# Kernel tuning notes

Hardware: AMD Instinct MI355X
Metric: run time of the kernel (lower is better)

Reference implementation:

```python
import jax, jax.numpy as jnp
import numpy as np

B, N, K = 4, 1024, 512
HEADS, DH = 8, 64
HID = 2048
KAPPA = 1.0      # kappa_beta
ALPHA = 1e-3     # ffn_alpha (prior weight)
LAM = 1.0        # ffn_lambda_belief
NITER = 2        # ffn_n_iterations
EPS = 1e-8


def _ln(x, g, b):
    m = jnp.mean(x, axis=-1, keepdims=True)
    v = jnp.var(x, axis=-1, keepdims=True)
    return (x - m) * jax.lax.rsqrt(v + 1e-5) * g + b


def _transport(x, phi, G):
    # truncated exp(phi . G) applied to x without materializing (B,N,K,K)
    def Ax(y):
        return jnp.einsum('bng,gkl,bnl->bnk', phi, G, y)
    a1 = Ax(x)
    return x + a1 + 0.5 * Ax(a1)


def setup_inputs() -> dict:
    key = jax.random.key(0)
    ks = jax.random.split(key, 16)
    mu_q = jax.random.normal(ks[0], (B, N, K), dtype=jnp.float32)
    sigma_q = jax.random.uniform(ks[1], (B, N, K), minval=0.5, maxval=1.5, dtype=jnp.float32)
    phi = 0.1 * jax.random.normal(ks[2], (B, N, 3), dtype=jnp.float32)
    A = jax.random.normal(ks[3], (3, K, K), dtype=jnp.float32)
    generators = 0.05 * (A - jnp.transpose(A, (0, 2, 1)))  # antisymmetric Lie generators
    mask = jnp.broadcast_to(jnp.tril(jnp.ones((N, N), dtype=bool)), (B, N, N))  # causal
    mu_prior = jax.random.normal(ks[4], (B, N, K), dtype=jnp.float32)
    s = 0.02
    Wq = s * jax.random.normal(ks[5], (K, K), dtype=jnp.float32)
    Wk = s * jax.random.normal(ks[6], (K, K), dtype=jnp.float32)
    Wv = s * jax.random.normal(ks[7], (K, K), dtype=jnp.float32)
    Wo = s * jax.random.normal(ks[8], (K, K), dtype=jnp.float32)
    g1 = jnp.ones((K,), jnp.float32); be1 = jnp.zeros((K,), jnp.float32)
    g2 = jnp.ones((K,), jnp.float32); be2 = jnp.zeros((K,), jnp.float32)
    W1 = s * jax.random.normal(ks[9], (K, HID), dtype=jnp.float32)
    bh1 = jnp.zeros((HID,), jnp.float32)
    W2 = s * jax.random.normal(ks[10], (HID, K), dtype=jnp.float32)
    bh2 = jnp.zeros((K,), jnp.float32)
    lr = jnp.array(0.1, jnp.float32)  # learnable VFE step size
    return {'mu_q': mu_q, 'sigma_q': sigma_q, 'phi': phi, 'generators': generators,
            'mask': mask, 'mu_prior': mu_prior, 'Wq': Wq, 'Wk': Wk, 'Wv': Wv, 'Wo': Wo,
            'g1': g1, 'be1': be1, 'g2': g2, 'be2': be2,
            'W1': W1, 'bh1': bh1, 'W2': W2, 'bh2': bh2, 'lr': lr}


def reference(mu_q, sigma_q, phi, generators, mask, mu_prior,
              Wq, Wk, Wv, Wo, g1, be1, g2, be2, W1, bh1, W2, bh2, lr):
    # ---- attention sublayer ----
    mu_n = _ln(mu_q, g1, be1)
    mu_g = _transport(mu_n, phi, generators)  # transport to common frame

    def heads(x):  # (B,N,K) -> (B,H,N,Dh)
        return x.reshape(B, N, HEADS, DH).transpose(0, 2, 1, 3)

    q = heads(mu_g @ Wq)
    k = heads(mu_g @ Wk)
    v = heads(mu_g @ Wv)
    # diagonal covariance propagated through linear maps: var_out = sigma @ W^2
    sq = heads(sigma_q @ (Wq * Wq)) + EPS
    sk = heads(sigma_q @ (Wk * Wk)) + EPS

    inv = 1.0 / sq
    # KL(N(k_j,sk_j) || N(q_i,sq_i)) for diagonal Gaussians, decomposed into matmuls
    tr = jnp.einsum('bhid,bhjd->bhij', inv, sk)
    quad = (jnp.sum(q * q * inv, axis=-1)[..., None]
            - 2.0 * jnp.einsum('bhid,bhjd->bhij', q * inv, k)
            + jnp.einsum('bhid,bhjd->bhij', inv, k * k))
    logdet = (jnp.sum(jnp.log(sq), axis=-1)[..., None]
              - jnp.sum(jnp.log(sk), axis=-1)[:, :, None, :])
    kl = 0.5 * (tr + quad - DH + logdet)  # (B,H,N,N)

    scores = jnp.where(mask[:, None, :, :], -kl / KAPPA, -1e9)
    beta = jax.nn.softmax(scores, axis=-1)

    out = jnp.einsum('bhij,bhjd->bhid', beta, v)
    out = out.transpose(0, 2, 1, 3).reshape(B, N, K)
    mu_attn = _transport(out @ Wo, -phi, generators)  # back-transport to local frames
    mu_res = mu_q + mu_attn  # residual (dropout is identity in eval)

    # ---- VFE_dynamic FFN sublayer ----
    mu_n2 = _ln(mu_res, g2, be2)
    beta_m = jnp.mean(beta, axis=1)  # (B,N,N) attention-belief coupling
    h = mu_n2
    for _ in range(NITER):
        drive = jax.nn.gelu(h @ W1 + bh1) @ W2 + bh2
        grad = ALPHA * (h - mu_prior) + LAM * (h - jnp.einsum('bij,bjk->bik', beta_m, h))
        h = h + lr * (drive - grad)
    mu_out = mu_res + (h - mu_n2)

    return (mu_out, sigma_q, phi)
```

## Files before the change

kernel.cpp:

```cpp
#include <hip/hip_runtime.h>
#include <math.h>

#define BB 4
#define NN 1024
#define KK 512
#define HH 8
#define DHh 64
#define HIDd 2048
#define BN (BB*NN)

typedef unsigned short u16;
typedef __attribute__((ext_vector_type(8))) short bf16x8;
typedef __attribute__((ext_vector_type(4))) float f32x4;

__device__ __forceinline__ float gelu_tanh(float x){
    float u = 0.7978845608028654f*(x + 0.044715f*x*x*x);
    u = fminf(fmaxf(u, -15.f), 15.f);
    float t = __expf(2.f*u);
    return x*t/(t+1.f);
}
__device__ __forceinline__ u16 f2bf(float x){
    unsigned int u = __float_as_uint(x);
    unsigned int r = (u + 0x7fffu + ((u>>16)&1u)) >> 16;
    return (u16)r;
}
__device__ __forceinline__ float bf2f(u16 b){
    return __uint_as_float(((unsigned int)b)<<16);
}
__device__ __forceinline__ void gload16(const void* g, void* l){
    __builtin_amdgcn_global_load_lds((__attribute__((address_space(1))) void*)g,
                                     (__attribute__((address_space(3))) void*)l, 16, 0, 0);
}
__device__ __forceinline__ void wsplit(u16* hi, u16* lo, size_t o, float v){
    u16 h = f2bf(v);
    hi[o] = h;
    if (lo) lo[o] = f2bf(v - bf2f(h));
}

__global__ __launch_bounds__(256) void split_t_k(
    const float* __restrict__ src, u16* __restrict__ hi, u16* __restrict__ lo,
    int Kc, int Nc, long sS, long sD, int square)
{
    __shared__ float t[32][33];
    const int n0 = blockIdx.x*32, k0 = blockIdx.y*32, bz = blockIdx.z;
    const float* S = src + (long)bz*sS;
    const int tx = threadIdx.x & 31, ty = threadIdx.x >> 5;
    for (int r = ty; r < 32; r += 8){
        float v = S[(long)(k0+r)*Nc + n0+tx];
        if (square) v *= v;
        t[r][tx] = v;
    }
    __syncthreads();
    for (int r = ty; r < 32; r += 8){
        float v = t[tx][r];
        long o = (long)bz*sD + (long)(n0+r)*Kc + k0 + tx;
        wsplit(hi, lo, o, v);
    }
}

__global__ __launch_bounds__(256) void wmega_k(
    const float* __restrict__ Wq, const float* __restrict__ Wk,
    const float* __restrict__ Wv, const float* __restrict__ Wo,
    const float* __restrict__ W1, const float* __restrict__ W2,
    const float* __restrict__ gen,
    u16* __restrict__ WQKVh, u16* __restrict__ WQKVl, u16* __restrict__ WoTh,
    u16* __restrict__ WSQKh, u16* __restrict__ WSQKl,
    u16* __restrict__ W1Th, u16* __restrict__ W2Th, u16* __restrict__ GFh)
{
    const int z = blockIdx.z;
    const int tid = threadIdx.x;
    if (z == 8){
        if (blockIdx.x >= 48) return;
        const int c0 = blockIdx.x*32, k0 = blockIdx.y*32;
        const int tx = tid&31, ty = tid>>5;
        const int g = c0/KK, l0 = c0%KK;
        for (int r=ty; r<32; r+=8)
            GFh[(size_t)(k0+r)*(3*KK) + c0+tx] =
                f2bf(gen[(size_t)g*KK*KK + (size_t)(k0+r)*KK + l0+tx]);
        return;
    }
    __shared__ float t[32][33];
    const float* src; u16* hi; u16* lo=0; int sq=0;
    int n0, k0, Kc, Nc;
    const size_t KK2 = (size_t)KK*KK;
    if (z < 6){
        if (blockIdx.x >= 16) return;
        n0 = blockIdx.x*32; k0 = blockIdx.y*32; Kc=KK; Nc=KK;
        if      (z==0){ src=Wq; hi=WQKVh;       lo=WQKVl; }
        else if (z==1){ src=Wk; hi=WQKVh+KK2;   lo=WQKVl+KK2; }
        else if (z==2){ src=Wv; hi=WQKVh+2*KK2; lo=WQKVl+2*KK2; }
        else if (z==3){ src=Wo; hi=WoTh; }
        else if (z==4){ src=Wq; hi=WSQKh;       lo=WSQKl; sq=1; }
        else          { src=Wk; hi=WSQKh+KK2;   lo=WSQKl+KK2; sq=1; }
    } else if (z == 6){
        src=W1; hi=W1Th; Kc=KK; Nc=HIDd;
        n0 = blockIdx.x*32; k0 = blockIdx.y*32;
    } else {
        src=W2; hi=W2Th; Kc=HIDd; Nc=KK;
        n0 = blockIdx.y*32; k0 = blockIdx.x*32;
    }
    const int tx=tid&31, ty=tid>>5;
    for (int r=ty;r<32;r+=8){
        float v = src[(long)(k0+r)*Nc + n0+tx];
        if (sq) v*=v;
        t[r][tx]=v;
    }
    __syncthreads();
    for (int r=ty;r<32;r+=8){
        float v = t[tx][r];
        long o = (long)(n0+r)*Kc + k0+tx;
        wsplit(hi, lo, o, v);
    }
}

__global__ __launch_bounds__(256) void gemm_mfma_k(
    const u16* __restrict__ Ah, const u16* __restrict__ Bh,
    float* __restrict__ C, u16* __restrict__ Chi, u16* __restrict__ Clo,
    int M, int Kc, int Nc, int lda,
    long sA, long sB, long sC, const float* __restrict__ bias, int act,
    int swz)
{
    __shared__ u16 shA[3][128*32], shB[3][128*32];
    int bx = blockIdx.x, by = blockIdx.y;
    if (swz){
        int lin = bx + gridDim.x*by;
        int within = lin & 31, st = lin >> 5;
        int stm = gridDim.x >> 3;
        bx = (st % stm)*8 + (within & 7);
        by = (st / stm)*4 + (within >> 3);
    }
    const int m0 = bx*128, n0 = by*128;
    const int bz = blockIdx.z;
    const u16* gAh = Ah + (long)bz*sA;
    const u16* gBh = Bh + (long)bz*sB;
    const int tid = threadIdx.x;
    const int wave = tid >> 6, lane = tid & 63;
    const int quad = lane >> 4, r16 = lane & 15;
    const int wm = (wave>>1)*64, wn = (wave&1)*64;

    f32x4 acc[4][4];
    #pragma unroll
    for (int i=0;i<4;i++)
        #pragma unroll
        for (int j=0;j<4;j++) acc[i][j] = (f32x4){0.f,0.f,0.f,0.f};

    auto stage = [&](int sel, int k0){
        #pragma unroll
        for (int half=0; half<2; ++half){
            int c = half*256 + tid;
            int row = c >> 2;
            int kg = ((c & 3) ^ ((row >> 1) & 3))*8;
            gload16(gAh + (long)(m0+row)*lda + k0 + kg, &shA[sel][c*8]);
            gload16(gBh + (long)(n0+row)*Kc  + k0 + kg, &shB[sel][c*8]);
        }
    };

    const int nsteps = Kc >> 5;
    stage(0, 0);
    if (1 < nsteps) stage(1, 1<<5);
    const int swr = (quad ^ ((r16 >> 1) & 3))*8;
    for (int t = 0; t < nsteps; ++t){
        if (t+1 < nsteps) asm volatile("s_waitcnt vmcnt(4)" ::: "memory");
        else              asm volatile("s_waitcnt vmcnt(0)" ::: "memory");
        __builtin_amdgcn_s_barrier();
        if (t+2 < nsteps) stage((t+2)%3, (t+2)<<5);
        const int rd = t % 3;
        bf16x8 afh[4], bfh[4];
        #pragma unroll
        for (int i=0;i<4;i++){
            afh[i] = *(const bf16x8*)&shA[rd][(wm+i*16+r16)*32 + swr];
            bfh[i] = *(const bf16x8*)&shB[rd][(wn+i*16+r16)*32 + swr];
        }
        #pragma unroll
        for (int i=0;i<4;i++)
            #pragma unroll
            for (int j=0;j<4;j++)
                acc[i][j] = __builtin_amdgcn_mfma_f32_16x16x32_bf16(afh[i], bfh[j], acc[i][j], 0,0,0);
    }
    #pragma unroll
    for (int i=0;i<4;i++){
        #pragma unroll
        for (int j=0;j<4;j++){
            int gc = n0 + wn + j*16 + r16;
            if (gc >= Nc) continue;
            float bv = bias ? bias[gc] : 0.f;
            #pragma unroll
            for (int r=0;r<4;r++){
                long gr = m0 + wm + i*16 + quad*4 + r;
                float v = acc[i][j][r] + bv;
                if (act) v = gelu_tanh(v);
                long o = (long)bz*sC + gr*Nc + gc;
                if (C) C[o] = v;
                if (Chi){ u16 t = f2bf(v); Chi[o] = t; if (Clo) Clo[o] = f2bf(v - bf2f(t)); }
            }
        }
    }
}

template<int NBUF>
__global__ __launch_bounds__(256) void gemm_v3_k(
    const u16* __restrict__ Ah, const u16* __restrict__ Al,
    const u16* __restrict__ Bh, const u16* __restrict__ Bl,
    float* __restrict__ C,
    int M, int Kc, int Nc, int lda,
    long sA, long sB, long sC, int cskip, int swzmode,
    const u16* __restrict__ Ah2, const u16* __restrict__ Al2,
    const u16* __restrict__ Bh2, const u16* __restrict__ Bl2,
    float* __restrict__ C2, int ycut, int Nc2)
{
    __shared__ u16 shA[NBUF][128*32], shB[NBUF][128*32];
    int bx = blockIdx.x, by = blockIdx.y, bz = blockIdx.z;
    if (swzmode == 1){
        int lin = bx + gridDim.x*by;
        int within = lin & 31, st = lin >> 5;
        int stm = gridDim.x >> 3;
        bx = (st % stm)*8 + (within & 7);
        by = (st / stm)*4 + (within >> 3);
    } else if (swzmode == 2){
        int lin = bx + gridDim.x*(by + gridDim.y*bz);
        int xcd = lin & 7, idx = lin >> 3;
        bz = xcd + 8*(idx >> 6);
        int tile = idx & 63;
        bx = tile & 7; by = tile >> 3;
    }
    if (ycut && by >= ycut){
        Ah = Ah2; Al = Al2; Bh = Bh2; Bl = Bl2; C = C2;
        by -= ycut; Nc = Nc2;
    }
    const int m0 = bx*128, n0 = by*128;
    if (cskip == 1 && n0 > m0 + 127) return;
    const u16* gAh = Ah + (long)bz*sA;
    const u16* gAl = Al + (long)bz*sA;
    const u16* gBh = Bh + (long)bz*sB;
    const u16* gBl = Bl + (long)bz*sB;
    const int tid = threadIdx.x;
    const int wave = tid >> 6, lane = tid & 63;
    const int quad = lane >> 4, r16 = lane & 15;
    const int wm = (wave>>1)*64, wn = (wave&1)*64;

    f32x4 acc[4][4];
    #pragma unroll
    for (int i=0;i<4;i++)
        #pragma unroll
        for (int j=0;j<4;j++) acc[i][j] = (f32x4){0.f,0.f,0.f,0.f};

    const int segsteps = Kc >> 5;
    const int nsteps = 3*segsteps;
    auto stage = [&](int sel, int t){
        int seg = (t >= segsteps) + (t >= 2*segsteps);
        int k0 = (t - seg*segsteps) << 5;
        const u16* a = (seg==1) ? gAl : gAh;
        const u16* b = (seg==2) ? gBl : gBh;
        #pragma unroll
        for (int half=0; half<2; ++half){
            int c = half*256 + tid;
            int row = c >> 2;
            int kg = ((c & 3) ^ ((row >> 1) & 3))*8;
            gload16(a + (long)(m0+row)*lda + k0 + kg, &shA[sel][c*8]);
            gload16(b + (long)(n0+row)*Kc  + k0 + kg, &shB[sel][c*8]);
        }
    };

    const int swr = (quad ^ ((r16 >> 1) & 3))*8;
    if constexpr (NBUF == 2){
        stage(0, 0);
        __syncthreads();
        int cur = 0;
        for (int t = 0; t < nsteps; ++t){
            if (t+1 < nsteps) stage(cur^1, t+1);
            bf16x8 afh[4], bfh[4];
            #pragma unroll
            for (int i=0;i<4;i++){
                afh[i] = *(const bf16x8*)&shA[cur][(wm+i*16+r16)*32 + swr];
                bfh[i] = *(const bf16x8*)&shB[cur][(wn+i*16+r16)*32 + swr];
            }
            #pragma unroll
            for (int i=0;i<4;i++)
                #pragma unroll
                for (int j=0;j<4;j++)
                    acc[i][j] = __builtin_amdgcn_mfma_f32_16x16x32_bf16(afh[i], bfh[j], acc[i][j], 0,0,0);
            __syncthreads();
            cur ^= 1;
        }
    } else {
        stage(0, 0);
        if (1 < nsteps) stage(1, 1);
        for (int t = 0; t < nsteps; ++t){
            if (t+1 < nsteps) asm volatile("s_waitcnt vmcnt(4)" ::: "memory");
            else              asm volatile("s_waitcnt vmcnt(0)" ::: "memory");
            __builtin_amdgcn_s_barrier();
            if (t+2 < nsteps) stage((t+2)%3, t+2);
            const int rd = t % 3;
            bf16x8 afh[4], bfh[4];
            #pragma unroll
            for (int i=0;i<4;i++){
                afh[i] = *(const bf16x8*)&shA[rd][(wm+i*16+r16)*32 + swr];
                bfh[i] = *(const bf16x8*)&shB[rd][(wn+i*16+r16)*32 + swr];
            }
            #pragma unroll
            for (int i=0;i<4;i++)
                #pragma unroll
                for (int j=0;j<4;j++)
                    acc[i][j] = __builtin_amdgcn_mfma_f32_16x16x32_bf16(afh[i], bfh[j], acc[i][j], 0,0,0);
        }
    }
    #pragma unroll
    for (int i=0;i<4;i++){
        #pragma unroll
        for (int j=0;j<4;j++){
            int gc = n0 + wn + j*16 + r16;
            if (gc >= Nc) continue;
            #pragma unroll
            for (int r=0;r<4;r++){
                long gr = m0 + wm + i*16 + quad*4 + r;
                if (cskip == 1 && gc > gr) continue;
                long o = (long)bz*sC + gr*Nc + gc;
                C[o] = acc[i][j][r];
            }
        }
    }
}

__global__ __launch_bounds__(256) void tgemm_k(
    const u16* __restrict__ Ahh,
    const u16* __restrict__ GFh,
    const float* __restrict__ phi, float esign,
    float* __restrict__ C, u16* __restrict__ Chi, u16* __restrict__ Clo,
    const float* __restrict__ t_x, const float* __restrict__ t_a1,
    const float* __restrict__ t_res)
{
    __shared__ u16 shA[2][64*64], shB[2][64*64];
    const int m0 = blockIdx.x*64, n0 = blockIdx.y*64;
    const int tid = threadIdx.x;
    const int wave = tid >> 6, lane = tid & 63;
    const int quad = lane >> 4, r16 = lane & 15;
    const int wr = wave*16;

    float ph[3][4];
    #pragma unroll
    for (int sgi=0; sgi<3; ++sgi)
        #pragma unroll
        for (int r=0; r<4; ++r)
            ph[sgi][r] = esign*phi[(size_t)(m0+wr+quad*4+r)*3 + sgi];

    f32x4 acc[4], tot[4];
    #pragma unroll
    for (int j=0;j<4;j++){ acc[j] = (f32x4){0.f,0.f,0.f,0.f}; tot[j] = acc[j]; }

    auto stage = [&](int sel, int t){
        int seg = t >> 3, k0 = (t & 7) << 6;
        #pragma unroll
        for (int rep=0; rep<2; ++rep){
            int c = rep*256 + tid;
            int row = c >> 3;
            int kg = ((c & 7) ^ (row & 7))*8;
            gload16(Ahh + (long)(m0+row)*KK + k0 + kg, &shA[sel][c*8]);
            gload16(GFh + (long)(n0+row)*(3*KK) + seg*KK + k0 + kg, &shB[sel][c*8]);
        }
    };

    stage(0, 0);
    __syncthreads();
    int cur = 0;
    for (int t = 0; t < 24; ++t){
        if (t+1 < 24) stage(cur^1, t+1);
        #pragma unroll
        for (int kk=0; kk<2; ++kk){
            const int s = (((kk<<2)+quad) ^ (r16 & 7))*8;
            bf16x8 af = *(const bf16x8*)&shA[cur][(wr+r16)*64 + s];
            #pragma unroll
            for (int j=0;j<4;j++){
                bf16x8 bh = *(const bf16x8*)&shB[cur][(j*16+r16)*64 + s];
                acc[j] = __builtin_amdgcn_mfma_f32_16x16x32_bf16(af, bh, acc[j], 0,0,0);
            }
        }
        if ((t & 7) == 7){
            int sgi = t >> 3;
            #pragma unroll
            for (int j=0;j<4;j++){
                #pragma unroll
                for (int r=0;r<4;r++) tot[j][r] += ph[sgi][r]*acc[j][r];
                acc[j] = (f32x4){0.f,0.f,0.f,0.f};
            }
        }
        __syncthreads();
        cur ^= 1;
    }
    #pragma unroll
    for (int j=0;j<4;j++){
        int gc = n0 + j*16 + r16;
        #pragma unroll
        for (int r=0;r<4;r++){
            long gr = m0 + wr + quad*4 + r;
            float v = tot[j][r];
            long o = gr*(long)KK + gc;
            if (t_x){
                v = t_x[o] + t_a1[o] + 0.5f*v;
                if (t_res) v += t_res[o];
            }
            if (C) C[o] = v;
            if (Chi){ u16 t2 = f2bf(v); Chi[o] = t2; if (Clo) Clo[o] = f2bf(v - bf2f(t2)); }
        }
    }
}

__global__ __launch_bounds__(256) void gemm64_k(
    const u16* __restrict__ Ah, const u16* __restrict__ Bh,
    float* __restrict__ C, u16* __restrict__ Chi, u16* __restrict__ Clo,
    int M, int Kc, int Nc, int lda,
    long sA, long sB, long sC, const float* __restrict__ bias, int act,
    int ktrim, int swz,
    const float* __restrict__ f_hin, const float* __restrict__ f_bmh,
    const float* __restrict__ f_mup, const float* __restrict__ f_lr,
    u16* __restrict__ f_hh, float* __restrict__ f_hout,
    const float* __restrict__ f_mrb, const float* __restrict__ f_mn2,
    float* __restrict__ f_out, int fmode)
{
    __shared__ u16 shA[2][64*64], shB[2][64*64];
    int bx = blockIdx.x, by = blockIdx.y;
    if (swz){
        int lin = bx + gridDim.x*by;
        int within = lin & 31, st = lin >> 5;
        int stm = gridDim.x >> 3;
        bx = (st % stm)*8 + (within & 7);
        by = (st / stm)*4 + (within >> 3);
    }
    const int m0 = bx*64, n0 = by*64;
    const int bz = blockIdx.z;
    const u16* gA = Ah + (long)bz*sA;
    const u16* gB = Bh + (long)bz*sB;
    const int tid = threadIdx.x;
    const int wave = tid >> 6, lane = tid & 63;
    const int quad = lane >> 4, r16 = lane & 15;
    const int wr = wave*16;
    const int kend = ktrim ? min(Kc, m0 + 64) : Kc;
    const int nsteps = kend >> 6;

    f32x4 acc[4];
    #pragma unroll
    for (int j=0;j<4;j++) acc[j] = (f32x4){0.f,0.f,0.f,0.f};

    auto stage = [&](int sel, int k0){
        #pragma unroll
        for (int rep=0; rep<2; ++rep){
            int c = rep*256 + tid;
            int row = c >> 3;
            int kg = ((c & 7) ^ (row & 7))*8;
            gload16(gA + (long)(m0+row)*lda + k0 + kg, &shA[sel][c*8]);
            gload16(gB + (long)(n0+row)*Kc + k0 + kg, &shB[sel][c*8]);
        }
    };

    stage(0, 0);
    __syncthreads();
    int cur = 0;
    for (int t = 0; t < nsteps; ++t){
        if (t+1 < nsteps) stage(cur^1, (t+1)<<6);
        #pragma unroll
        for (int kk=0; kk<2; ++kk){
            const int s = (((kk<<2)+quad) ^ (r16 & 7))*8;
            bf16x8 af = *(const bf16x8*)&shA[cur][(wr+r16)*64 + s];
            #pragma unroll
            for (int j=0;j<4;j++){
                bf16x8 bh = *(const bf16x8*)&shB[cur][(j*16+r16)*64 + s];
                acc[j] = __builtin_amdgcn_mfma_f32_16x16x32_bf16(af, bh, acc[j], 0,0,0);
            }
        }
        __syncthreads();
        cur ^= 1;
    }
    float lrv = 0.f;
    if (fmode) lrv = *f_lr;
    #pragma unroll
    for (int j=0;j<4;j++){
        int gc = n0 + j*16 + r16;
        float bv = bias ? bias[gc] : 0.f;
        #pragma unroll
        for (int r=0;r<4;r++){
            long gr = m0 + wr + quad*4 + r;
            float v = acc[j][r] + bv;
            if (act) v = gelu_tanh(v);
            long o = (long)bz*sC + gr*Nc + gc;
            if (fmode){
                float hv = f_hin[o];
                float val = hv + lrv*(v - (1e-3f*(hv - f_mup[o]) + (hv - f_bmh[o])));
                if (fmode == 1){ f_hout[o] = val; f_hh[o] = f2bf(val); }
                else           { f_out[o] = f_mrb[o] + val - f_mn2[o]; }
            } else {
                if (C) C[o] = v;
                if (Chi){ u16 t = f2bf(v); Chi[o] = t; if (Clo) Clo[o] = f2bf(v - bf2f(t)); }
            }
        }
    }
}

__global__ __launch_bounds__(256) void ln_k(
    const float* __restrict__ x, const float* __restrict__ g,
    const float* __restrict__ be, float* __restrict__ y,
    u16* __restrict__ yh16,
    const float* __restrict__ sg, u16* __restrict__ sgh, u16* __restrict__ sgl,
    float* __restrict__ osig, const float* __restrict__ phi, float* __restrict__ ophi)
{
    __shared__ float sh[8];
    const int r = blockIdx.x, tid = threadIdx.x;
    const float* xr = x + (long)r*KK;
    float2 v = *(const float2*)(xr + tid*2);
    float s = v.x+v.y, s2 = v.x*v.x+v.y*v.y;
    #pragma unroll
    for (int o=32;o>0;o>>=1){ s += __shfl_down(s,o); s2 += __shfl_down(s2,o); }
    if ((tid&63)==0){ sh[tid>>6]=s; sh[4+(tid>>6)]=s2; }
    __syncthreads();
    s  = sh[0]+sh[1]+sh[2]+sh[3];
    s2 = sh[4]+sh[5]+sh[6]+sh[7];
    const float mean = s*(1.f/KK);
    const float var  = s2*(1.f/KK) - mean*mean;
    const float rs = rsqrtf(var + 1e-5f);
    float2 gg = *(const float2*)(g + tid*2);
    float2 bb = *(const float2*)(be + tid*2);
    float ox = (v.x-mean)*rs*gg.x + bb.x;
    float oy = (v.y-mean)*rs*gg.y + bb.y;
    long o = (long)r*KK + tid*2;
    *(float2*)(y + o) = make_float2(ox, oy);
    if (yh16){ yh16[o] = f2bf(ox); yh16[o+1] = f2bf(oy); }
    if (sgh){
        float2 sv = *(const float2*)(sg + o);
        wsplit(sgh, sgl, o,   sv.x);
        wsplit(sgh, sgl, o+1, sv.y);
        if (osig) *(float2*)(osig + o) = sv;
    }
    if (ophi && tid < 3) ophi[(size_t)r*3 + tid] = phi[(size_t)r*3 + tid];
}

__global__ __launch_bounds__(512) void prepvt_k(
    const float* __restrict__ QKV, const float* __restrict__ SQSK,
    u16* __restrict__ CFh, u16* __restrict__ CFl,
    u16* __restrict__ KSh, u16* __restrict__ KSl, float* __restrict__ dvec,
    u16* __restrict__ VTh)
{
    __shared__ float t[64][65];
    const int bx = blockIdx.x;
    const int tid = threadIdx.x;
    if (bx < BN){
        const int bn = bx;
        const int b = bn / NN, n = bn % NN;
        const int h = tid >> 6, d = tid & 63;
        float q  = QKV[(size_t)bn*1536 + h*DHh + d];
        float k  = QKV[(size_t)bn*1536 + KK + h*DHh + d];
        float sq = SQSK[(size_t)bn*1024 + h*DHh + d] + 1e-8f;
        float sk = SQSK[(size_t)bn*1024 + KK + h*DHh + d] + 1e-8f;
        float inv = 1.f/sq;
        float nqi = -2.f*q*inv;
        float skk = sk + k*k;
        const size_t base = ((size_t)(h*BB + b)*NN + n)*128;
        wsplit(CFh, CFl, base+d,    inv);
        wsplit(CFh, CFl, base+64+d, nqi);
        wsplit(KSh, KSl, base+d,    skk);
        wsplit(KSh, KSl, base+64+d, k);
        float dv = __logf(sk);
        #pragma unroll
        for (int o=32;o>0;o>>=1) dv += __shfl_down(dv,o);
        if (d==0) dvec[((size_t)h*BB + b)*NN + n] = dv;
        return;
    }
    const int idx = bx - BN;
    const int n0 = (idx & 15)*64;
    const int h = (idx>>4)&7;
    const int b = idx>>7;
    const int c4 = (tid & 15) * 4;
    const int r0 = tid >> 4;
    for (int rr = r0; rr < 64; rr += 32){
        float4 v = *(const float4*)(QKV + (size_t)(b*NN + n0 + rr)*1536 + 1024 + h*DHh + c4);
        t[c4+0][rr] = v.x; t[c4+1][rr] = v.y; t[c4+2][rr] = v.z; t[c4+3][rr] = v.w;
    }
    __syncthreads();
    for (int dd = r0; dd < 64; dd += 32){
        size_t base = ((size_t)(h*BB + b)*64 + dd)*NN + n0 + c4;
        #pragma unroll
        for (int q=0;q<4;q++) VTh[base+q] = f2bf(t[dd][c4+q]);
    }
}

__global__ __launch_bounds__(256) void softmax_all_k(
    float* __restrict__ S, const float* __restrict__ dvec, u16* __restrict__ BMh)
{
    __shared__ float s_redA[2][4], s_redB[2][4];
    const int tid = threadIdx.x;
    const int b = blockIdx.x >> 10, i = blockIdx.x & (NN-1);
    const int L = i + 1;
    const int JEND = ((i >> 6) + 1) << 6;
    const int j4 = tid*4;
    const bool act = (j4 < JEND);
    const int wv = tid >> 6;
    const bool lane0 = ((tid & 63) == 0);

    float bm[4] = {0.f,0.f,0.f,0.f};
    float4 rv = make_float4(0,0,0,0), dpv = make_float4(0,0,0,0);
    if (act){
        rv  = *(const float4*)(S + ((long)(0*BB + b)*NN + i)*NN + j4);
        dpv = *(const float4*)(dvec + (size_t)(0*BB + b)*NN + j4);
    }
    for (int h = 0; h < 8; ++h){
        const int z = h*BB + b;
        float4 rvn = make_float4(0,0,0,0), dpn = make_float4(0,0,0,0);
        if (h < 7 && act){
            const int zn = (h+1)*BB + b;
            rvn = *(const float4*)(S + ((long)zn*NN + i)*NN + j4);
            dpn = *(const float4*)(dvec + (size_t)zn*NN + j4);
        }
        float sc[4];
        const float* rp = (const float*)&rv;
        const float* dp = (const float*)&dpv;
        #pragma unroll
        for (int e=0;e<4;e++){
            float s = -0.5f*rp[e] + 0.5f*dp[e];
            sc[e] = (act && (j4 + e < L)) ? s : -3.0e38f;
        }
        float lm = fmaxf(fmaxf(sc[0],sc[1]), fmaxf(sc[2],sc[3]));
        #pragma unroll
        for (int o=32;o>0;o>>=1) lm = fmaxf(lm, __shfl_xor(lm, o));
        if (lane0) s_redA[h&1][wv] = lm;
        __syncthreads();
        const float mx = fmaxf(fmaxf(s_redA[h&1][0],s_redA[h&1][1]),
                               fmaxf(s_redA[h&1][2],s_redA[h&1][3]));
        float w4[4], ps = 0.f;
        #pragma unroll
        for (int e=0;e<4;e++){
            float e1 = (act && (j4 + e < L)) ? __expf(sc[e]-mx) : 0.f;
            w4[e] = e1; ps += e1;
        }
        #pragma unroll
        for (int o=32;o>0;o>>=1) ps += __shfl_xor(ps, o);
        if (lane0) s_redB[h&1][wv] = ps;
        __syncthreads();
        const float isum = 1.f/(s_redB[h&1][0]+s_redB[h&1][1]+s_redB[h&1][2]+s_redB[h&1][3]);
        if (act){
            u16* brow = (u16*)(S + ((long)z*NN + i)*NN);
            ushort4 st;
            float w0=w4[0]*isum, w1=w4[1]*isum, w2=w4[2]*isum, w3=w4[3]*isum;
            bm[0]+=0.125f*w0; bm[1]+=0.125f*w1; bm[2]+=0.125f*w2; bm[3]+=0.125f*w3;
            st.x=f2bf(w0); st.y=f2bf(w1); st.z=f2bf(w2); st.w=f2bf(w3);
            *(ushort4*)(brow + j4) = st;
        }
        rv = rvn; dpv = dpn;
    }
    if (act){
        const long bmrow = ((long)b*NN + i)*NN;
        ushort4 st;
        st.x=f2bf(bm[0]); st.y=f2bf(bm[1]); st.z=f2bf(bm[2]); st.w=f2bf(bm[3]);
        *(ushort4*)(BMh + bmrow + j4) = st;
    }
}

__global__ __launch_bounds__(256) void pv_k(
    const u16* __restrict__ Sbeta,
    const u16* __restrict__ VTh,
    u16* __restrict__ xh)
{
    __shared__ u16 shA[2][64*64], shB[2][64*64];
    const int m0 = blockIdx.x*64;
    const int z = blockIdx.y;
    const int b = z & 3, head = z >> 2;
    const int tid = threadIdx.x;
    const int wave = tid>>6, lane = tid&63;
    const int quad = lane>>4, r16 = lane&15;
    f32x4 acc[4];
    #pragma unroll
    for (int j=0;j<4;j++) acc[j]=(f32x4){0.f,0.f,0.f,0.f};
    const int nsteps = (m0 >> 6) + 1;

    auto stage = [&](int sel, int j0){
        #pragma unroll
        for (int rep=0; rep<2; ++rep){
            int c = rep*256 + tid;
            int row = c >> 3;
            int k8 = ((c & 7) ^ (row & 7))*8;
            gload16(Sbeta + ((size_t)(z*NN + m0 + row))*(2*NN) + j0 + k8, &shA[sel][c*8]);
            gload16(VTh + ((size_t)(z*64 + row))*NN + j0 + k8, &shB[sel][c*8]);
        }
    };

    stage(0, 0);
    __syncthreads();
    int cur = 0;
    for (int t = 0; t < nsteps; ++t){
        if (t+1 < nsteps) stage(cur^1, (t+1)<<6);
        #pragma unroll
        for (int kk=0; kk<2; ++kk){
            const int s = (((kk<<2)+quad) ^ (r16 & 7))*8;
            bf16x8 af = *(const bf16x8*)&shA[cur][(wave*16 + r16)*64 + s];
            #pragma unroll
            for (int nj=0; nj<4; ++nj){
                bf16x8 bh = *(const bf16x8*)&shB[cur][(nj*16 + r16)*64 + s];
                acc[nj] = __builtin_amdgcn_mfma_f32_16x16x32_bf16(af, bh, acc[nj], 0,0,0);
            }
        }
        __syncthreads();
        cur ^= 1;
    }
    #pragma unroll
    for (int nj=0;nj<4;nj++){
        #pragma unroll
        for (int r=0;r<4;r++){
            int i = m0 + wave*16 + quad*4 + r;
            int d = nj*16 + r16;
            size_t o = ((size_t)(b*NN)+i)*KK + head*64 + d;
            xh[o] = f2bf(acc[nj][r]);
        }
    }
}

extern "C" void kernel_launch(void* const* d_in, const int* in_sizes, int n_in,
                              void* d_out, int out_size, void* d_ws, size_t ws_size,
                              hipStream_t stream) {
    const float* mu_q    = (const float*)d_in[0];
    const float* sigma_q = (const float*)d_in[1];
    const float* phi     = (const float*)d_in[2];
    const float* gen     = (const float*)d_in[3];
    const float* mu_prior= (const float*)d_in[5];
    const float* Wq = (const float*)d_in[6];
    const float* Wk = (const float*)d_in[7];
    const float* Wv = (const float*)d_in[8];
    const float* Wo = (const float*)d_in[9];
    const float* g1 = (const float*)d_in[10];
    const float* be1= (const float*)d_in[11];
    const float* g2 = (const float*)d_in[12];
    const float* be2= (const float*)d_in[13];
    const float* W1 = (const float*)d_in[14];
    const float* bh1= (const float*)d_in[15];
    const float* W2 = (const float*)d_in[16];
    const float* bh2= (const float*)d_in[17];
    const float* lr = (const float*)d_in[18];
    float* out = (float*)d_out;

    float* w = (float*)d_ws;
    size_t off = 0;
    auto alloc = [&](size_t n){ float* p = w + off; off += (n+3)&~(size_t)3; return p; };
    auto ualloc = [&](size_t n){ return (u16*)alloc((n+1)/2); };

    float* Xb   = alloc((size_t)BN*KK);
    float* A1b  = alloc((size_t)BN*KK);
    float* A2b  = alloc((size_t)BN*KK);
    float* QKVb = alloc((size_t)BN*3*KK);
    float* SQSKb= alloc((size_t)BN*2*KK);
    float* REG  = alloc((size_t)16*NN*NN);
    float* Sbig = Xb;
    u16*  SGh   = (u16*)REG;
    u16*  SGl   = SGh + (size_t)BN*KK;
    u16*  Xh    = SGl + (size_t)BN*KK;
    u16*  A1h   = Xh  + (size_t)BN*KK;
    u16*  WOh   = A1h + (size_t)BN*KK;
    u16*  ZH    = (u16*)REG;
    float* Db_  = alloc((size_t)HH*BB*NN);
    u16* AH  = ualloc((size_t)BN*HIDd); u16* AL  = ualloc((size_t)BN*HIDd);
    u16* CFh = AH;
    u16* CFl = AH + (size_t)HH*BB*NN*128;
    u16* KSh = AL;
    u16* KSl = AL + (size_t)HH*BB*NN*128;
    u16* VTh = ualloc((size_t)HH*BB*64*NN);
    u16* GFh = ualloc((size_t)3*KK*KK);
    u16* WQKVh= ualloc((size_t)3*KK*KK); u16* WQKVl= ualloc((size_t)3*KK*KK);
    u16* WSQKh= ualloc((size_t)2*KK*KK); u16* WSQKl= ualloc((size_t)2*KK*KK);
    u16* WoTh= ualloc((size_t)KK*KK);
    u16* W1Th= ualloc((size_t)KK*HIDd);
    u16* W2Th= ualloc((size_t)KK*HIDd);
    u16* BMh = ualloc((size_t)BB*NN*NN);
    u16* HTh = ualloc((size_t)BB*KK*NN);
    float* WOb = QKVb;
    float* Hb  = QKVb + (size_t)BN*KK;
    float* MRb = QKVb + 2*(size_t)BN*KK;
    float* MN2b= Xb;
    (void)A2b;

    {
        dim3 gw(64, 16, 9);
        wmega_k<<<gw, 256, 0, stream>>>(Wq, Wk, Wv, Wo, W1, W2, gen,
                                        WQKVh, WQKVl, WoTh, WSQKh, WSQKl,
                                        W1Th, W2Th, GFh);
    }

    ln_k<<<BN, 256, 0, stream>>>(mu_q, g1, be1, Xb, Xh, sigma_q, SGh, SGl,
                                 out + (size_t)BN*KK, phi, out + 2*(size_t)BN*KK);
    {
        dim3 tg(BN/64, KK/64, 1);
        tgemm_k<<<tg, 256, 0, stream>>>(Xh, GFh, phi, 1.f, A1b, A1h, 0, 0, 0, 0);
        tgemm_k<<<tg, 256, 0, stream>>>(A1h, GFh, phi, 1.f, 0, AH, AL, Xb, A1b, 0);
    }

    {
        dim3 g(BN/128, 20, 1);
        gemm_v3_k<3><<<g, 256, 0, stream>>>(AH, AL, WQKVh, WQKVl, QKVb,
            BN, KK, 3*KK, KK, 0, 0, 0, 0, 1,
            SGh, SGl, WSQKh, WSQKl, SQSKb, 12, 2*KK);
    }
    prepvt_k<<<BN + 512, 512, 0, stream>>>(QKVb, SQSKb, CFh, CFl, KSh, KSl, Db_, VTh);

    {
        dim3 sg(NN/128, NN/128, 32);
        gemm_v3_k<2><<<sg, 256, 0, stream>>>(CFh, CFl, KSh, KSl, Sbig,
            NN, 128, NN, 128, (long)NN*128, (long)NN*128, (long)NN*NN, 1, 2,
            0, 0, 0, 0, 0, 0, 0);
        softmax_all_k<<<BB*NN, 256, 0, stream>>>(Sbig, Db_, BMh);
        dim3 pg(NN/64, 32, 1);
        pv_k<<<pg, 256, 0, stream>>>((const u16*)Sbig, VTh, AH);
    }

    {
        dim3 wg(BN/64, KK/64, 1);
        gemm64_k<<<wg, 256, 0, stream>>>(AH, WoTh, WOb, WOh, 0,
            BN, KK, KK, KK, 0,0,0, nullptr, 0, 0, 0,
            0,0,0,0,0,0,0,0,0,0);
        dim3 tg(BN/64, KK/64, 1);
        tgemm_k<<<tg, 256, 0, stream>>>(WOh, GFh, phi, -1.f, A1b, A1h, 0, 0, 0, 0);
        tgemm_k<<<tg, 256, 0, stream>>>(A1h, GFh, phi, -1.f, MRb, 0, 0, WOb, A1b, mu_q);
    }
    ln_k<<<BN, 256, 0, stream>>>(MRb, g2, be2, MN2b, AH, 0, 0, 0, 0, 0, 0);

    for (int it=0; it<2; ++it){
        const float* hin = (it==0) ? MN2b : Hb;
        {
            dim3 tg(KK/32, NN/32, BB);
            split_t_k<<<tg, 256, 0, stream>>>(hin, HTh, 0, NN, KK,
                                              (long)NN*KK, (long)KK*NN, 0);
        }
        {
            dim3 bg(NN/64, KK/64, BB);
            gemm64_k<<<bg, 256, 0, stream>>>(BMh, HTh, A1b, 0,0,
                                             NN, NN, KK, NN,
                                             (long)NN*NN, (long)KK*NN, (long)NN*KK,
                                             nullptr, 0, 1, 0,
                                             0,0,0,0,0,0,0,0,0,0);
        }
        {
            dim3 wg1(BN/128, HIDd/128, 1);
            gemm_mfma_k<<<wg1, 256, 0, stream>>>(AH, W1Th, 0, ZH, 0,
                BN, KK, HIDd, KK, 0, 0, 0, bh1, 1, 1);
        }
        {
            dim3 wg(BN/64, KK/64, 1);
            gemm64_k<<<wg, 256, 0, stream>>>(ZH, W2Th, 0,0,0,
                                             BN, HIDd, KK, HIDd, 0,0,0, bh2, 0, 0, 1,
                                             hin, A1b, mu_prior, lr, AH, Hb, MRb, MN2b, out,
                                             (it==0) ? 1 : 2);
        }
    }

    (void)in_sizes; (void)n_in; (void)out_size; (void)ws_size;
}
```

Measured before the change: 554.5 us.

## Fuse belief-coupling GEMM into W1 GEMM launch and fold score scaling into epilogue

The beta_m @ h causal batched GEMM is merged into the W1 MFMA GEMM launch as extra grid rows (ycut), with the K range truncated to the causal bound so masked blocks are skipped. The KL score affine transform (-0.5*S + 0.5*d) moves into the QK GEMM epilogue, so softmax no longer reads the dvec array. Softmax now writes zero-filled beta_m out to a 128-aligned bound so the truncated GEMM reads valid zeros. Together these remove one kernel launch per iteration and cut softmax memory traffic, at the cost of mixed-workload blocks in one grid whose K lengths differ.

```diff
diff --git a/kernel.cpp b/kernel.cpp
--- a/kernel.cpp
+++ b/kernel.cpp
@@ -118,7 +118,9 @@
     float* __restrict__ C, u16* __restrict__ Chi, u16* __restrict__ Clo,
     int M, int Kc, int Nc, int lda,
     long sA, long sB, long sC, const float* __restrict__ bias, int act,
-    int swz)
+    int swz,
+    const u16* __restrict__ A2, const u16* __restrict__ B2,
+    float* __restrict__ C2, int ycut)
 {
     __shared__ u16 shA[3][128*32], shB[3][128*32];
     int bx = blockIdx.x, by = blockIdx.y;
@@ -129,10 +131,24 @@
         bx = (st % stm)*8 + (within & 7);
         by = (st / stm)*4 + (within >> 3);
     }
-    const int m0 = bx*128, n0 = by*128;
-    const int bz = blockIdx.z;
-    const u16* gAh = Ah + (long)bz*sA;
-    const u16* gBh = Bh + (long)bz*sB;
+    int bz = blockIdx.z;
+    int m0, n0, kend;
+    const u16 *gAh, *gBh;
+    if (ycut && by < ycut){
+        m0 = (bx & 7)*128; n0 = by*128; bz = bx >> 3;
+        gAh = A2 + (long)bz*NN*NN;
+        gBh = B2 + (long)bz*KK*NN;
+        Kc = NN; lda = NN; Nc = KK;
+        C = C2 + (long)bz*NN*KK; Chi = 0; Clo = 0; bias = 0; act = 0; sC = 0;
+        kend = m0 + 128;
+        bz = 0;
+    } else {
+        if (ycut) by -= ycut;
+        m0 = bx*128; n0 = by*128;
+        gAh = Ah + (long)bz*sA;
+        gBh = Bh + (long)bz*sB;
+        kend = Kc;
+    }
     const int tid = threadIdx.x;
     const int wave = tid >> 6, lane = tid & 63;
     const int quad = lane >> 4, r16 = lane & 15;
@@ -155,7 +171,7 @@
         }
     };
 
-    const int nsteps = Kc >> 5;
+    const int nsteps = kend >> 5;
     stage(0, 0);
     if (1 < nsteps) stage(1, 1<<5);
     const int swr = (quad ^ ((r16 >> 1) & 3))*8;
@@ -206,7 +222,8 @@
     long sA, long sB, long sC, int cskip, int swzmode,
     const u16* __restrict__ Ah2, const u16* __restrict__ Al2,
     const u16* __restrict__ Bh2, const u16* __restrict__ Bl2,
-    float* __restrict__ C2, int ycut, int Nc2)
+    float* __restrict__ C2, int ycut, int Nc2,
+    const float* __restrict__ dvec)
 {
     __shared__ u16 shA[NBUF][128*32], shB[NBUF][128*32];
     int bx = blockIdx.x, by = blockIdx.y, bz = blockIdx.z;
@@ -304,6 +321,12 @@
                     acc[i][j] = __builtin_amdgcn_mfma_f32_16x16x32_bf16(afh[i], bfh[j], acc[i][j], 0,0,0);
         }
     }
+    float dv4[4];
+    if (dvec){
+        #pragma unroll
+        for (int j=0;j<4;j++)
+            dv4[j] = 0.5f*dvec[(size_t)bz*NN + n0 + wn + j*16 + r16];
+    }
     #pragma unroll
     for (int i=0;i<4;i++){
         #pragma unroll
@@ -315,7 +338,9 @@
                 long gr = m0 + wm + i*16 + quad*4 + r;
                 if (cskip == 1 && gc > gr) continue;
                 long o = (long)bz*sC + gr*Nc + gc;
-                C[o] = acc[i][j][r];
+                float v = acc[i][j][r];
+                if (dvec) v = -0.5f*v + dv4[j];
+                C[o] = v;
             }
         }
     }
@@ -581,40 +606,34 @@
 }
 
 __global__ __launch_bounds__(256) void softmax_all_k(
-    float* __restrict__ S, const float* __restrict__ dvec, u16* __restrict__ BMh)
+    float* __restrict__ S, u16* __restrict__ BMh)
 {
     __shared__ float s_redA[2][4], s_redB[2][4];
     const int tid = threadIdx.x;
     const int b = blockIdx.x >> 10, i = blockIdx.x & (NN-1);
     const int L = i + 1;
     const int JEND = ((i >> 6) + 1) << 6;
+    const int JEND2 = ((i >> 7) + 1) << 7;
     const int j4 = tid*4;
     const bool act = (j4 < JEND);
     const int wv = tid >> 6;
     const bool lane0 = ((tid & 63) == 0);
 
     float bm[4] = {0.f,0.f,0.f,0.f};
-    float4 rv = make_float4(0,0,0,0), dpv = make_float4(0,0,0,0);
-    if (act){
-        rv  = *(const float4*)(S + ((long)(0*BB + b)*NN + i)*NN + j4);
-        dpv = *(const float4*)(dvec + (size_t)(0*BB + b)*NN + j4);
-    }
+    float4 rv = make_float4(0,0,0,0);
+    if (act) rv = *(const float4*)(S + ((long)(0*BB + b)*NN + i)*NN + j4);
     for (int h = 0; h < 8; ++h){
         const int z = h*BB + b;
-        float4 rvn = make_float4(0,0,0,0), dpn = make_float4(0,0,0,0);
+        float4 rvn = make_float4(0,0,0,0);
         if (h < 7 && act){
             const int zn = (h+1)*BB + b;
             rvn = *(const float4*)(S + ((long)zn*NN + i)*NN + j4);
-            dpn = *(const float4*)(dvec + (size_t)zn*NN + j4);
         }
         float sc[4];
         const float* rp = (const float*)&rv;
-        const float* dp = (const float*)&dpv;
-        #pragma unroll
-        for (int e=0;e<4;e++){
-            float s = -0.5f*rp[e] + 0.5f*dp[e];
-            sc[e] = (act && (j4 + e < L)) ? s : -3.0e38f;
-        }
+        #pragma unroll
+        for (int e=0;e<4;e++)
+            sc[e] = (act && (j4 + e < L)) ? rp[e] : -3.0e38f;
         float lm = fmaxf(fmaxf(sc[0],sc[1]), fmaxf(sc[2],sc[3]));
         #pragma unroll
         for (int o=32;o>0;o>>=1) lm = fmaxf(lm, __shfl_xor(lm, o));
@@ -641,9 +660,9 @@
             st.x=f2bf(w0); st.y=f2bf(w1); st.z=f2bf(w2); st.w=f2bf(w3);
             *(ushort4*)(brow + j4) = st;
         }
-        rv = rvn; dpv = dpn;
-    }
-    if (act){
+        rv = rvn;
+    }
+    if (j4 < JEND2){
         const long bmrow = ((long)b*NN + i)*NN;
         ushort4 st;
         st.x=f2bf(bm[0]); st.y=f2bf(bm[1]); st.z=f2bf(bm[2]); st.w=f2bf(bm[3]);
@@ -790,7 +809,7 @@
         dim3 g(BN/128, 20, 1);
         gemm_v3_k<3><<<g, 256, 0, stream>>>(AH, AL, WQKVh, WQKVl, QKVb,
             BN, KK, 3*KK, KK, 0, 0, 0, 0, 1,
-            SGh, SGl, WSQKh, WSQKl, SQSKb, 12, 2*KK);
+            SGh, SGl, WSQKh, WSQKl, SQSKb, 12, 2*KK, 0);
     }
     prepvt_k<<<BN + 512, 512, 0, stream>>>(QKVb, SQSKb, CFh, CFl, KSh, KSl, Db_, VTh);
 
@@ -798,8 +817,8 @@
         dim3 sg(NN/128, NN/128, 32);
         gemm_v3_k<2><<<sg, 256, 0, stream>>>(CFh, CFl, KSh, KSl, Sbig,
             NN, 128, NN, 128, (long)NN*128, (long)NN*128, (long)NN*NN, 1, 2,
-            0, 0, 0, 0, 0, 0, 0);
-        softmax_all_k<<<BB*NN, 256, 0, stream>>>(Sbig, Db_, BMh);
+            0, 0, 0, 0, 0, 0, 0, Db_);
+        softmax_all_k<<<BB*NN, 256, 0, stream>>>(Sbig, BMh);
         dim3 pg(NN/64, 32, 1);
         pv_k<<<pg, 256, 0, stream>>>((const u16*)Sbig, VTh, AH);
     }
@@ -823,17 +842,10 @@
                                               (long)NN*KK, (long)KK*NN, 0);
         }
         {
-            dim3 bg(NN/64, KK/64, BB);
-            gemm64_k<<<bg, 256, 0, stream>>>(BMh, HTh, A1b, 0,0,
-                                             NN, NN, KK, NN,
-                                             (long)NN*NN, (long)KK*NN, (long)NN*KK,
-                                             nullptr, 0, 1, 0,
-                                             0,0,0,0,0,0,0,0,0,0);
-        }
-        {
-            dim3 wg1(BN/128, HIDd/128, 1);
+            dim3 wg1(BN/128, 4 + HIDd/128, 1);
             gemm_mfma_k<<<wg1, 256, 0, stream>>>(AH, W1Th, 0, ZH, 0,
-                BN, KK, HIDd, KK, 0, 0, 0, bh1, 1, 1);
+                BN, KK, HIDd, KK, 0, 0, 0, bh1, 1, 1,
+                BMh, HTh, A1b, 4);
         }
         {
             dim3 wg(BN/64, KK/64, 1);
```

Result: faster. 540.8 us (-2.5%).
